# Kernel optimization log

Hardware: AMD Instinct MI355X
Metric: run time of the kernel (lower is better)

The kernel has to match this reference:

```python
import jax, jax.numpy as jnp
import numpy as np

BS = 4096
D_M = 256
D_D = 1024
D_INNER = 2 * D_D            # 2048
DT_RANK = 16                 # ceil(256/16)
D_STATE = 16


def setup_inputs() -> dict:
    key = jax.random.key(0)
    ks = jax.random.split(key, 10)
    bbox = jax.random.normal(ks[0], (BS, 4), dtype=jnp.float32)
    hidden_state = jax.random.normal(ks[1], (BS, D_INNER, D_STATE), dtype=jnp.float32)
    flow_embed = jax.random.normal(ks[2], (BS, D_M), dtype=jnp.float32)
    # parameters
    W_in = jax.random.normal(ks[3], (D_INNER * 2, 4), dtype=jnp.float32) * 0.02
    b_in = jnp.zeros((D_INNER * 2,), dtype=jnp.float32)
    dt_init_std = DT_RANK ** (-0.5)
    W_dt = jax.random.uniform(ks[4], (D_INNER, DT_RANK), dtype=jnp.float32,
                              minval=-dt_init_std, maxval=dt_init_std)
    # dt bias init (inverse softplus of dt sampled log-uniform in [1e-3, 1e-1])
    dt = jnp.exp(jax.random.uniform(ks[5], (D_INNER,)) * (np.log(0.1) - np.log(0.001)) + np.log(0.001))
    dt = jnp.clip(dt, 1e-4, None)
    b_dt = dt + jnp.log(-jnp.expm1(-dt))
    W_flow = jax.random.normal(ks[6], (DT_RANK + 2 * D_STATE, D_M), dtype=jnp.float32) * 0.02
    A_log = jnp.log(jnp.broadcast_to(jnp.arange(1, D_STATE + 1, dtype=jnp.float32), (D_INNER, D_STATE)))
    D = jnp.ones((D_INNER,), dtype=jnp.float32)
    W_out = jax.random.normal(ks[7], (4, D_INNER), dtype=jnp.float32) * 0.02
    b_out = jnp.zeros((4,), dtype=jnp.float32)
    return dict(bbox=bbox, hidden_state=hidden_state, flow_embed=flow_embed,
                W_in=W_in, b_in=b_in, W_dt=W_dt, b_dt=b_dt, W_flow=W_flow,
                A_log=A_log, D=D, W_out=W_out, b_out=b_out)


def reference(bbox, hidden_state, flow_embed, W_in, b_in, W_dt, b_dt, W_flow,
              A_log, D, W_out, b_out):
    # in_proj and gating split
    bbox_hdim = bbox @ W_in.T + b_in                 # (bs, 2*d_inner)
    e_i, r_i = jnp.split(bbox_hdim, 2, axis=-1)      # each (bs, d_inner)
    e_i = jax.nn.silu(e_i)
    A = -jnp.exp(A_log.astype(jnp.float32))          # (d_inner, d_state)
    # flow projection -> dt, B, C
    proj_f = flow_embed @ W_flow.T                   # (bs, dt_rank + 2*d_state)
    dt, B, C = jnp.split(proj_f, [DT_RANK, DT_RANK + D_STATE], axis=-1)
    dt = dt @ W_dt.T                                 # (bs, d_inner)
    dt = jax.nn.softplus(dt + b_dt)
    # selective state update
    dA = jnp.exp(jnp.einsum('bd,dn->bdn', dt, A))    # (bs, d_inner, d_state)
    dB = jnp.einsum('bd,bn->bdn', dt, B)
    hidden_state = hidden_state * dA + e_i[:, :, None] * dB
    y = jnp.einsum('bdn,bn->bd', hidden_state, C)
    y = y + D * e_i
    y = y * jax.nn.silu(r_i)
    out = y @ W_out.T + b_out                        # (bs, 4)
    return out, hidden_state
```

## Files before the change

### kernel.cpp

```cpp
#include <hip/hip_runtime.h>
#include <math.h>

#define BS      4096
#define DM      256
#define DINNER  2048
#define DSTATE  16

__device__ __forceinline__ float silu_f(float x) {
    return x / (1.f + __expf(-x));
}

__device__ __forceinline__ float softplus_f(float x) {
    if (x > 20.f) return x;
    if (x < -20.f) return __expf(x);
    return __logf(1.f + __expf(x));
}

__global__ void a_precompute_kernel(const float* __restrict__ A_log,
                                    float* __restrict__ A) {
    int i = blockIdx.x * 256 + threadIdx.x;
    A[i] = -__expf(A_log[i]);
}

__global__ __launch_bounds__(256)
void flow_main_kernel(const float* __restrict__ bbox,
                      const float* __restrict__ h_in,
                      const float* __restrict__ flow_embed,
                      const float* __restrict__ W_in,
                      const float* __restrict__ b_in,
                      const float* __restrict__ W_dt,
                      const float* __restrict__ b_dt,
                      const float* __restrict__ W_flow,
                      const float* __restrict__ Aptr,
                      int a_ready,
                      const float* __restrict__ Dvec,
                      const float* __restrict__ W_out,
                      const float* __restrict__ b_out,
                      float* __restrict__ out,
                      float* __restrict__ h_out)
{
    __shared__ __align__(16) float fe_s[DM];
    __shared__ float proj_s[48];
    __shared__ float pp_s[48][4];
    __shared__ float dt_s[DINNER];
    __shared__ float edt_s[DINNER];
    __shared__ float ye_s[DINNER];
    __shared__ float rs_s[DINNER];
    __shared__ float red_s[4][4];

    const int b = blockIdx.x;
    const int t = threadIdx.x;

    fe_s[t] = flow_embed[b * DM + t];
    __syncthreads();

    if (t < 192) {
        const int k = t >> 2, p = t & 3;
        const float4* wf  = (const float4*)(W_flow + k * DM);
        const float4* fe4 = (const float4*)fe_s;
        float s = 0.f;
        #pragma unroll
        for (int i = 0; i < 16; ++i) {
            float4 w = wf[p * 16 + i];
            float4 f = fe4[p * 16 + i];
            s += w.x * f.x + w.y * f.y + w.z * f.z + w.w * f.w;
        }
        pp_s[k][p] = s;
    }
    __syncthreads();
    if (t < 48)
        proj_s[t] = pp_s[t][0] + pp_s[t][1] + pp_s[t][2] + pp_s[t][3];
    __syncthreads();

    float dl[16];
    #pragma unroll
    for (int k = 0; k < 16; ++k) dl[k] = proj_s[k];
    const float4 bb = ((const float4*)bbox)[b];

    #pragma unroll
    for (int i = 0; i < 8; ++i) {
        const int d = t + i * 256;
        float4 wi = ((const float4*)W_in)[d];
        float e = fmaf(bb.x, wi.x, fmaf(bb.y, wi.y, fmaf(bb.z, wi.z, bb.w * wi.w))) + b_in[d];
        e = silu_f(e);
        float4 wr = ((const float4*)W_in)[DINNER + d];
        float r = fmaf(bb.x, wr.x, fmaf(bb.y, wr.y, fmaf(bb.z, wr.z, bb.w * wr.w))) + b_in[DINNER + d];
        const float rs = silu_f(r);

        const float4* wd = (const float4*)(W_dt + d * 16);
        float s = 0.f;
        #pragma unroll
        for (int j = 0; j < 4; ++j) {
            float4 w = wd[j];
            s += w.x * dl[j * 4 + 0] + w.y * dl[j * 4 + 1] +
                 w.z * dl[j * 4 + 2] + w.w * dl[j * 4 + 3];
        }
        const float dt = softplus_f(s + b_dt[d]);

        dt_s[d]  = dt;
        edt_s[d] = e * dt;
        ye_s[d]  = Dvec[d] * e;
        rs_s[d]  = rs;
    }
    __syncthreads();

    const int nq = t & 3;
    float Bq[4], Cq[4];
    #pragma unroll
    for (int j = 0; j < 4; ++j) {
        Bq[j] = proj_s[16 + nq * 4 + j];
        Cq[j] = proj_s[32 + nq * 4 + j];
    }

    const float4* __restrict__ hin4  = (const float4*)(h_in + (size_t)b * 32768);
    float4* __restrict__       hout4 = (float4*)(h_out + (size_t)b * 32768);
    const float4* __restrict__ A4    = (const float4*)Aptr;

    float acc0 = 0.f, acc1 = 0.f, acc2 = 0.f, acc3 = 0.f;

    #pragma unroll 2
    for (int it = 0; it < 32; ++it) {
        const int idx = it * 256 + t;
        const int d   = idx >> 2;
        float4 h = hin4[idx];
        float4 a = A4[idx];
        if (!a_ready) {
            a.x = -__expf(a.x); a.y = -__expf(a.y);
            a.z = -__expf(a.z); a.w = -__expf(a.w);
        }
        const float dt  = dt_s[d];
        const float edt = edt_s[d];
        float4 hn;
        hn.x = fmaf(h.x, __expf(dt * a.x), edt * Bq[0]);
        hn.y = fmaf(h.y, __expf(dt * a.y), edt * Bq[1]);
        hn.z = fmaf(h.z, __expf(dt * a.z), edt * Bq[2]);
        hn.w = fmaf(h.w, __expf(dt * a.w), edt * Bq[3]);
        hout4[idx] = hn;

        float ys = hn.x * Cq[0] + hn.y * Cq[1] + hn.z * Cq[2] + hn.w * Cq[3];
        ys += __shfl_xor(ys, 1, 64);
        ys += __shfl_xor(ys, 2, 64);
        if (nq == 0) {
            const float y = (ys + ye_s[d]) * rs_s[d];
            acc0 = fmaf(y, W_out[d],          acc0);
            acc1 = fmaf(y, W_out[DINNER + d], acc1);
            acc2 = fmaf(y, W_out[2 * DINNER + d], acc2);
            acc3 = fmaf(y, W_out[3 * DINNER + d], acc3);
        }
    }

    #pragma unroll
    for (int off = 4; off < 64; off <<= 1) {
        acc0 += __shfl_xor(acc0, off, 64);
        acc1 += __shfl_xor(acc1, off, 64);
        acc2 += __shfl_xor(acc2, off, 64);
        acc3 += __shfl_xor(acc3, off, 64);
    }
    const int wave = t >> 6;
    if ((t & 63) == 0) {
        red_s[wave][0] = acc0; red_s[wave][1] = acc1;
        red_s[wave][2] = acc2; red_s[wave][3] = acc3;
    }
    __syncthreads();
    if (t == 0) {
        #pragma unroll
        for (int j = 0; j < 4; ++j) {
            out[b * 4 + j] = red_s[0][j] + red_s[1][j] + red_s[2][j] + red_s[3][j]
                           + b_out[j];
        }
    }
}

extern "C" void kernel_launch(void* const* d_in, const int* in_sizes, int n_in,
                              void* d_out, int out_size, void* d_ws, size_t ws_size,
                              hipStream_t stream) {
    const float* bbox   = (const float*)d_in[0];
    const float* h_in   = (const float*)d_in[1];
    const float* fe     = (const float*)d_in[2];
    const float* W_in   = (const float*)d_in[3];
    const float* b_in   = (const float*)d_in[4];
    const float* W_dt   = (const float*)d_in[5];
    const float* b_dt   = (const float*)d_in[6];
    const float* W_flow = (const float*)d_in[7];
    const float* A_log  = (const float*)d_in[8];
    const float* Dvec   = (const float*)d_in[9];
    const float* W_out  = (const float*)d_in[10];
    const float* b_out  = (const float*)d_in[11];

    float* out   = (float*)d_out;
    float* h_out = out + BS * 4;

    const size_t a_bytes = (size_t)DINNER * DSTATE * sizeof(float);
    const int a_ready = (ws_size >= a_bytes) ? 1 : 0;
    const float* Aptr = A_log;
    if (a_ready) {
        float* Aws = (float*)d_ws;
        hipLaunchKernelGGL(a_precompute_kernel, dim3((DINNER * DSTATE) / 256),
                           dim3(256), 0, stream, A_log, Aws);
        Aptr = Aws;
    }

    hipLaunchKernelGGL(flow_main_kernel, dim3(BS), dim3(256), 0, stream,
                       bbox, h_in, fe, W_in, b_in, W_dt, b_dt, W_flow,
                       Aptr, a_ready, Dvec, W_out, b_out, out, h_out);
}
```

Before: 973.8 us.

## Assign one d_inner row per thread and fuse prologue into state update

Each thread now handles a whole d_inner row (all 16 states) and computes e, r, dt on the fly. This removes the shared-memory staging arrays, the block barrier and the quad shuffles. Stores to h_out are nontemporal, and launch bounds request 4 blocks per CU. The catch is that each thread now reads 256 contiguous bytes, so a wave's loads are strided rather than coalesced across lanes. Register pressure also rises from the 48 per-thread scalars and 8 unrolled rows.

```diff
diff --git a/kernel.cpp b/kernel.cpp
--- a/kernel.cpp
+++ b/kernel.cpp
@@ -6,6 +6,8 @@
 #define DINNER  2048
 #define DSTATE  16
 
+typedef float f32x4 __attribute__((ext_vector_type(4)));
+
 __device__ __forceinline__ float silu_f(float x) {
     return x / (1.f + __expf(-x));
 }
@@ -16,13 +18,17 @@
     return __logf(1.f + __expf(x));
 }
 
+__device__ __forceinline__ float rfl(float x) {
+    return __int_as_float(__builtin_amdgcn_readfirstlane(__float_as_int(x)));
+}
+
 __global__ void a_precompute_kernel(const float* __restrict__ A_log,
                                     float* __restrict__ A) {
     int i = blockIdx.x * 256 + threadIdx.x;
     A[i] = -__expf(A_log[i]);
 }
 
-__global__ __launch_bounds__(256)
+__global__ __launch_bounds__(256, 4)
 void flow_main_kernel(const float* __restrict__ bbox,
                       const float* __restrict__ h_in,
                       const float* __restrict__ flow_embed,
@@ -40,12 +46,8 @@
                       float* __restrict__ h_out)
 {
     __shared__ __align__(16) float fe_s[DM];
-    __shared__ float proj_s[48];
     __shared__ float pp_s[48][4];
-    __shared__ float dt_s[DINNER];
-    __shared__ float edt_s[DINNER];
-    __shared__ float ye_s[DINNER];
-    __shared__ float rs_s[DINNER];
+    __shared__ __align__(16) float proj_s[48];
     __shared__ float red_s[4][4];
 
     const int b = blockIdx.x;
@@ -72,85 +74,104 @@
         proj_s[t] = pp_s[t][0] + pp_s[t][1] + pp_s[t][2] + pp_s[t][3];
     __syncthreads();
 
-    float dl[16];
+    float dl[16], Bn[16], Cn[16];
     #pragma unroll
-    for (int k = 0; k < 16; ++k) dl[k] = proj_s[k];
+    for (int n = 0; n < 16; ++n) {
+        dl[n] = rfl(proj_s[n]);
+        Bn[n] = rfl(proj_s[16 + n]);
+        Cn[n] = rfl(proj_s[32 + n]);
+    }
+
     const float4 bb = ((const float4*)bbox)[b];
-
-    #pragma unroll
-    for (int i = 0; i < 8; ++i) {
-        const int d = t + i * 256;
-        float4 wi = ((const float4*)W_in)[d];
-        float e = fmaf(bb.x, wi.x, fmaf(bb.y, wi.y, fmaf(bb.z, wi.z, bb.w * wi.w))) + b_in[d];
-        e = silu_f(e);
-        float4 wr = ((const float4*)W_in)[DINNER + d];
-        float r = fmaf(bb.x, wr.x, fmaf(bb.y, wr.y, fmaf(bb.z, wr.z, bb.w * wr.w))) + b_in[DINNER + d];
-        const float rs = silu_f(r);
-
-        const float4* wd = (const float4*)(W_dt + d * 16);
-        float s = 0.f;
-        #pragma unroll
-        for (int j = 0; j < 4; ++j) {
-            float4 w = wd[j];
-            s += w.x * dl[j * 4 + 0] + w.y * dl[j * 4 + 1] +
-                 w.z * dl[j * 4 + 2] + w.w * dl[j * 4 + 3];
-        }
-        const float dt = softplus_f(s + b_dt[d]);
-
-        dt_s[d]  = dt;
-        edt_s[d] = e * dt;
-        ye_s[d]  = Dvec[d] * e;
-        rs_s[d]  = rs;
-    }
-    __syncthreads();
-
-    const int nq = t & 3;
-    float Bq[4], Cq[4];
-    #pragma unroll
-    for (int j = 0; j < 4; ++j) {
-        Bq[j] = proj_s[16 + nq * 4 + j];
-        Cq[j] = proj_s[32 + nq * 4 + j];
-    }
-
     const float4* __restrict__ hin4  = (const float4*)(h_in + (size_t)b * 32768);
     float4* __restrict__       hout4 = (float4*)(h_out + (size_t)b * 32768);
     const float4* __restrict__ A4    = (const float4*)Aptr;
 
     float acc0 = 0.f, acc1 = 0.f, acc2 = 0.f, acc3 = 0.f;
 
-    #pragma unroll 2
-    for (int it = 0; it < 32; ++it) {
-        const int idx = it * 256 + t;
-        const int d   = idx >> 2;
-        float4 h = hin4[idx];
-        float4 a = A4[idx];
+    #pragma unroll
+    for (int i = 0; i < 8; ++i) {
+        const int d = i * 256 + t;
+        const int q = d * 4;
+
+        float4 h0 = hin4[q + 0], h1 = hin4[q + 1], h2 = hin4[q + 2], h3 = hin4[q + 3];
+        float4 a0 = A4[q + 0],   a1 = A4[q + 1],   a2 = A4[q + 2],   a3 = A4[q + 3];
+
+        float4 wi = ((const float4*)W_in)[d];
+        float4 wr = ((const float4*)W_in)[DINNER + d];
+        const float4* wd = (const float4*)(W_dt + d * 16);
+        float4 w0 = wd[0], w1 = wd[1], w2 = wd[2], w3 = wd[3];
+        const float bi_e = b_in[d];
+        const float bi_r = b_in[DINNER + d];
+        const float bdt  = b_dt[d];
+        const float dd   = Dvec[d];
+        const float wo0  = W_out[d];
+        const float wo1  = W_out[DINNER + d];
+        const float wo2  = W_out[2 * DINNER + d];
+        const float wo3  = W_out[3 * DINNER + d];
+
+        float e = fmaf(bb.x, wi.x, fmaf(bb.y, wi.y, fmaf(bb.z, wi.z, bb.w * wi.w))) + bi_e;
+        e = silu_f(e);
+        float r = fmaf(bb.x, wr.x, fmaf(bb.y, wr.y, fmaf(bb.z, wr.z, bb.w * wr.w))) + bi_r;
+        const float rs = silu_f(r);
+
+        float s = w0.x * dl[0];
+        s = fmaf(w0.y, dl[1],  s); s = fmaf(w0.z, dl[2],  s); s = fmaf(w0.w, dl[3],  s);
+        s = fmaf(w1.x, dl[4],  s); s = fmaf(w1.y, dl[5],  s); s = fmaf(w1.z, dl[6],  s);
+        s = fmaf(w1.w, dl[7],  s); s = fmaf(w2.x, dl[8],  s); s = fmaf(w2.y, dl[9],  s);
+        s = fmaf(w2.z, dl[10], s); s = fmaf(w2.w, dl[11], s); s = fmaf(w3.x, dl[12], s);
+        s = fmaf(w3.y, dl[13], s); s = fmaf(w3.z, dl[14], s); s = fmaf(w3.w, dl[15], s);
+
+        const float dt  = softplus_f(s + bdt);
+        const float edt = e * dt;
+        const float ye  = dd * e;
+
         if (!a_ready) {
-            a.x = -__expf(a.x); a.y = -__expf(a.y);
-            a.z = -__expf(a.z); a.w = -__expf(a.w);
+            a0.x = -__expf(a0.x); a0.y = -__expf(a0.y); a0.z = -__expf(a0.z); a0.w = -__expf(a0.w);
+            a1.x = -__expf(a1.x); a1.y = -__expf(a1.y); a1.z = -__expf(a1.z); a1.w = -__expf(a1.w);
+            a2.x = -__expf(a2.x); a2.y = -__expf(a2.y); a2.z = -__expf(a2.z); a2.w = -__expf(a2.w);
+            a3.x = -__expf(a3.x); a3.y = -__expf(a3.y); a3.z = -__expf(a3.z); a3.w = -__expf(a3.w);
         }
-        const float dt  = dt_s[d];
-        const float edt = edt_s[d];
-        float4 hn;
-        hn.x = fmaf(h.x, __expf(dt * a.x), edt * Bq[0]);
-        hn.y = fmaf(h.y, __expf(dt * a.y), edt * Bq[1]);
-        hn.z = fmaf(h.z, __expf(dt * a.z), edt * Bq[2]);
-        hn.w = fmaf(h.w, __expf(dt * a.w), edt * Bq[3]);
-        hout4[idx] = hn;
-
-        float ys = hn.x * Cq[0] + hn.y * Cq[1] + hn.z * Cq[2] + hn.w * Cq[3];
-        ys += __shfl_xor(ys, 1, 64);
-        ys += __shfl_xor(ys, 2, 64);
-        if (nq == 0) {
-            const float y = (ys + ye_s[d]) * rs_s[d];
-            acc0 = fmaf(y, W_out[d],          acc0);
-            acc1 = fmaf(y, W_out[DINNER + d], acc1);
-            acc2 = fmaf(y, W_out[2 * DINNER + d], acc2);
-            acc3 = fmaf(y, W_out[3 * DINNER + d], acc3);
-        }
+
+        float4 hn0, hn1, hn2, hn3;
+        hn0.x = fmaf(h0.x, __expf(dt * a0.x), edt * Bn[0]);
+        hn0.y = fmaf(h0.y, __expf(dt * a0.y), edt * Bn[1]);
+        hn0.z = fmaf(h0.z, __expf(dt * a0.z), edt * Bn[2]);
+        hn0.w = fmaf(h0.w, __expf(dt * a0.w), edt * Bn[3]);
+        hn1.x = fmaf(h1.x, __expf(dt * a1.x), edt * Bn[4]);
+        hn1.y = fmaf(h1.y, __expf(dt * a1.y), edt * Bn[5]);
+        hn1.z = fmaf(h1.z, __expf(dt * a1.z), edt * Bn[6]);
+        hn1.w = fmaf(h1.w, __expf(dt * a1.w), edt * Bn[7]);
+        hn2.x = fmaf(h2.x, __expf(dt * a2.x), edt * Bn[8]);
+        hn2.y = fmaf(h2.y, __expf(dt * a2.y), edt * Bn[9]);
+        hn2.z = fmaf(h2.z, __expf(dt * a2.z), edt * Bn[10]);
+        hn2.w = fmaf(h2.w, __expf(dt * a2.w), edt * Bn[11]);
+        hn3.x = fmaf(h3.x, __expf(dt * a3.x), edt * Bn[12]);
+        hn3.y = fmaf(h3.y, __expf(dt * a3.y), edt * Bn[13]);
+        hn3.z = fmaf(h3.z, __expf(dt * a3.z), edt * Bn[14]);
+        hn3.w = fmaf(h3.w, __expf(dt * a3.w), edt * Bn[15]);
+
+        __builtin_nontemporal_store(*(const f32x4*)&hn0, (f32x4*)(hout4 + q + 0));
+        __builtin_nontemporal_store(*(const f32x4*)&hn1, (f32x4*)(hout4 + q + 1));
+        __builtin_nontemporal_store(*(const f32x4*)&hn2, (f32x4*)(hout4 + q + 2));
+        __builtin_nontemporal_store(*(const f32x4*)&hn3, (f32x4*)(hout4 + q + 3));
+
+        float ys = hn0.x * Cn[0];
+        ys = fmaf(hn0.y, Cn[1],  ys); ys = fmaf(hn0.z, Cn[2],  ys); ys = fmaf(hn0.w, Cn[3],  ys);
+        ys = fmaf(hn1.x, Cn[4],  ys); ys = fmaf(hn1.y, Cn[5],  ys); ys = fmaf(hn1.z, Cn[6],  ys);
+        ys = fmaf(hn1.w, Cn[7],  ys); ys = fmaf(hn2.x, Cn[8],  ys); ys = fmaf(hn2.y, Cn[9],  ys);
+        ys = fmaf(hn2.z, Cn[10], ys); ys = fmaf(hn2.w, Cn[11], ys); ys = fmaf(hn3.x, Cn[12], ys);
+        ys = fmaf(hn3.y, Cn[13], ys); ys = fmaf(hn3.z, Cn[14], ys); ys = fmaf(hn3.w, Cn[15], ys);
+
+        const float y = (ys + ye) * rs;
+        acc0 = fmaf(y, wo0, acc0);
+        acc1 = fmaf(y, wo1, acc1);
+        acc2 = fmaf(y, wo2, acc2);
+        acc3 = fmaf(y, wo3, acc3);
     }
 
     #pragma unroll
-    for (int off = 4; off < 64; off <<= 1) {
+    for (int off = 1; off < 64; off <<= 1) {
         acc0 += __shfl_xor(acc0, off, 64);
         acc1 += __shfl_xor(acc1, off, 64);
         acc2 += __shfl_xor(acc2, off, 64);
```

Result: slower. 1.419 ms (+45.7%).
